# Kernel optimization log

Measured on AMD Instinct MI355X. Metric: run time of the kernel, lower is better.

Reference implementation:

```python
import jax, jax.numpy as jnp
import numpy as np

DIM = 768
HEADS = 12
HIDDEN = 3072  # dim * mlp_ratio
EPS = 1e-5


def layernorm(x, g, b):
    mu = jnp.mean(x, axis=-1, keepdims=True)
    var = jnp.var(x, axis=-1, keepdims=True)
    return (x - mu) * jax.lax.rsqrt(var + EPS) * g + b


def setup_inputs() -> dict:
    key = jax.random.key(0)
    ks = jax.random.split(key, 10)
    s = 0.02
    return {
        "x": jax.random.normal(ks[0], (4, 1024, DIM), jnp.float32),
        "attention_mask": jax.random.randint(ks[1], (4, 1024), 0, 2, jnp.int32),
        "ln1_g": jnp.ones((DIM,), jnp.float32),
        "ln1_b": jnp.zeros((DIM,), jnp.float32),
        "ln2_g": jnp.ones((DIM,), jnp.float32),
        "ln2_b": jnp.zeros((DIM,), jnp.float32),
        "w_qkv": jax.random.normal(ks[2], (DIM, 3 * DIM), jnp.float32) * s,
        "b_qkv": jnp.zeros((3 * DIM,), jnp.float32),
        "w_proj": jax.random.normal(ks[3], (DIM, DIM), jnp.float32) * s,
        "b_proj": jnp.zeros((DIM,), jnp.float32),
        "w_fc1": jax.random.normal(ks[4], (DIM, HIDDEN), jnp.float32) * s,
        "b_fc1": jnp.zeros((HIDDEN,), jnp.float32),
        "w_fc2": jax.random.normal(ks[5], (HIDDEN, DIM), jnp.float32) * s,
        "b_fc2": jnp.zeros((DIM,), jnp.float32),
    }


def reference(x, attention_mask, ln1_g, ln1_b, ln2_g, ln2_b,
              w_qkv, b_qkv, w_proj, b_proj, w_fc1, b_fc1, w_fc2, b_fc2):
    B, N, C = x.shape
    hd = C // HEADS
    scale = hd ** -0.5

    # --- attention branch ---
    h = layernorm(x, ln1_g, ln1_b)
    qkv = (h @ w_qkv + b_qkv).reshape(B, N, 3, HEADS, hd)
    q, k, v = qkv[:, :, 0], qkv[:, :, 1], qkv[:, :, 2]  # [B,N,H,hd]
    attn = jnp.einsum('bnhd,bmhd->bhnm', q, k) * scale
    mask_bias = jnp.where(attention_mask == 0, -10000.0, 0.0)[:, None, None, :]
    attn = jax.nn.softmax(attn + mask_bias, axis=-1)
    o = jnp.einsum('bhnm,bmhd->bnhd', attn, v).reshape(B, N, C)
    x = x + (o @ w_proj + b_proj)

    # --- MLP branch ---
    h = layernorm(x, ln2_g, ln2_b)
    h = jax.nn.gelu(h @ w_fc1 + b_fc1, approximate=False)
    x = x + (h @ w_fc2 + b_fc2)
    return x
```

## Files before the change

### kernel.cpp

```cpp
#include <hip/hip_runtime.h>

#define DIM 768
#define NTOK 4096
#define HID 3072

typedef __attribute__((ext_vector_type(8))) short bf16x8;
typedef __attribute__((ext_vector_type(4))) float f32x4;

__device__ inline unsigned short f2bf(float f){
  unsigned u = __float_as_uint(f);
  u += 0x7fff + ((u >> 16) & 1);
  return (unsigned short)(u >> 16);
}
__device__ inline unsigned cvt_pk_bf16(float a, float b){
  unsigned r;
  asm("v_cvt_pk_bf16_f32 %0, %1, %2" : "=v"(r) : "v"(a), "v"(b));
  return r;
}
__device__ inline void gload_lds16(const void* g, void* l){
  __builtin_amdgcn_global_load_lds(
      (const __attribute__((address_space(1))) unsigned int*)g,
      (__attribute__((address_space(3))) unsigned int*)l, 16, 0, 0);
}
template<int N> __device__ inline void wait_vmcnt(){
  if constexpr (N == 0) asm volatile("s_waitcnt vmcnt(0)" ::: "memory");
  else if constexpr (N == 2) asm volatile("s_waitcnt vmcnt(2)" ::: "memory");
  else if constexpr (N == 3) asm volatile("s_waitcnt vmcnt(3)" ::: "memory");
  else if constexpr (N == 4) asm volatile("s_waitcnt vmcnt(4)" ::: "memory");
  else static_assert(N == 0, "unsupported vmcnt");
}

__global__ __launch_bounds__(256) void ln_kernel(const float* __restrict__ x,
    const float* __restrict__ g, const float* __restrict__ b,
    unsigned short* __restrict__ out)
{
  int row = blockIdx.x * 4 + (threadIdx.x >> 6);
  int lane = threadIdx.x & 63;
  const float* xr = x + (size_t)row * DIM;
  float4 v[3];
  float s = 0.f, s2 = 0.f;
#pragma unroll
  for (int j = 0; j < 3; ++j){
    v[j] = *(const float4*)(xr + j * 256 + lane * 4);
    s  += v[j].x + v[j].y + v[j].z + v[j].w;
    s2 += v[j].x*v[j].x + v[j].y*v[j].y + v[j].z*v[j].z + v[j].w*v[j].w;
  }
#pragma unroll
  for (int m = 1; m < 64; m <<= 1){ s += __shfl_xor(s, m, 64); s2 += __shfl_xor(s2, m, 64); }
  float mu  = s * (1.f / 768.f);
  float var = s2 * (1.f / 768.f) - mu * mu;
  float inv = rsqrtf(var + 1e-5f);
#pragma unroll
  for (int j = 0; j < 3; ++j){
    int c0 = j * 256 + lane * 4;
    float vv[4] = { v[j].x, v[j].y, v[j].z, v[j].w };
    ushort4 o4;
    o4.x = f2bf((vv[0] - mu) * inv * g[c0 + 0] + b[c0 + 0]);
    o4.y = f2bf((vv[1] - mu) * inv * g[c0 + 1] + b[c0 + 1]);
    o4.z = f2bf((vv[2] - mu) * inv * g[c0 + 2] + b[c0 + 2]);
    o4.w = f2bf((vv[3] - mu) * inv * g[c0 + 3] + b[c0 + 3]);
    *(ushort4*)(out + (size_t)row * DIM + c0) = o4;
  }
}

__global__ __launch_bounds__(256) void transpose4_kernel(
    const float* __restrict__ w_qkv, const float* __restrict__ w_proj,
    const float* __restrict__ w_fc1, const float* __restrict__ w_fc2,
    unsigned short* __restrict__ tq, unsigned short* __restrict__ tp,
    unsigned short* __restrict__ t1, unsigned short* __restrict__ t2)
{
  __shared__ __align__(16) unsigned short tile[32][33];
  int id = blockIdx.x;
  const float* W; unsigned short* Wt; int K, N, tx_n;
  if (id < 1728)      { W = w_qkv;  Wt = tq; K = 768;  N = 2304; tx_n = 72; }
  else if (id < 2304) { W = w_proj; Wt = tp; K = 768;  N = 768;  tx_n = 24; id -= 1728; }
  else if (id < 4608) { W = w_fc1;  Wt = t1; K = 768;  N = 3072; tx_n = 96; id -= 2304; }
  else                { W = w_fc2;  Wt = t2; K = 3072; N = 768;  tx_n = 24; id -= 4608; }
  int n0 = (id % tx_n) * 32, k0 = (id / tx_n) * 32;
  int tx = threadIdx.x & 31, ty = threadIdx.x >> 5;
#pragma unroll
  for (int i = 0; i < 32; i += 8)
    tile[ty + i][tx] = f2bf(W[(size_t)(k0 + ty + i) * N + n0 + tx]);
  __syncthreads();
#pragma unroll
  for (int i = 0; i < 32; i += 8)
    Wt[(size_t)(n0 + ty + i) * K + k0 + tx] = tile[tx][ty + i];
}

__global__ __launch_bounds__(256) void pack_mask_kernel(const int* __restrict__ am,
    unsigned long long* __restrict__ pm)
{
  int lane = threadIdx.x & 63, w = threadIdx.x >> 6, b = blockIdx.x;
  for (int k = w; k < 16; k += 4){
    unsigned long long m = __ballot(am[b * 1024 + k * 64 + lane] != 0);
    if (lane == 0) pm[b * 16 + k] = m;
  }
}

template<int BM, int BN, int WM, int WN, int EPI, typename OutT>
__global__ __launch_bounds__(256) void gemm_kernel(
    const unsigned short* __restrict__ A,
    const unsigned short* __restrict__ Bt,
    const float* __restrict__ bias,
    const float* __restrict__ resid,
    OutT* __restrict__ C,
    unsigned short* __restrict__ q_out,
    unsigned short* __restrict__ k_out,
    unsigned short* __restrict__ v_out,
    int M, int N, int K)
{
  constexpr int BK = 32;
  constexpr int WAVES_N = BN / WN;
  constexpr int MI = WM / 16, NI = WN / 16;
  constexpr int ACH = BM * BK / 8, BCH = BN * BK / 8;
  constexpr int NC = (ACH + BCH) / 256;
  constexpr int STAGE_B = 3 * (BM + BN) * BK * 2;
  constexpr int EPI_B = (EPI == 2) ? BM * (BN + 4) * 4 : BM * (BN + 8) * 2;
  constexpr int SMEM_B = STAGE_B > EPI_B ? STAGE_B : EPI_B;
  __shared__ __align__(16) char smem[SMEM_B];
  auto As = (unsigned short(*)[BM * BK])smem;
  auto Bs = (unsigned short(*)[BN * BK])(smem + 3 * BM * BK * 2);
  const int t = threadIdx.x, lane = t & 63, wid = t >> 6;
  const int lo = lane & 15, hi = lane >> 4;
  const int wr = wid / WAVES_N, wc = wid % WAVES_N;

  const int gx = gridDim.x;
  const int nwg = gx * gridDim.y;
  const int lin = blockIdx.y * gx + blockIdx.x;
  const int swz = (lin & 7) * (nwg >> 3) + (lin >> 3);
  const int bm = (swz / gx) * BM, bn = (swz % gx) * BN;

  auto stage = [&](int buf, int k0){
#pragma unroll
    for (int u = 0; u < NC; ++u){
      int c = u * 256 + t;
      if (c < ACH){
        gload_lds16(A + (size_t)(bm + (c >> 2)) * K + k0 + (c & 3) * 8, &As[buf][c * 8]);
      } else {
        int c2 = c - ACH;
        gload_lds16(Bt + (size_t)(bn + (c2 >> 2)) * K + k0 + (c2 & 3) * 8, &Bs[buf][c2 * 8]);
      }
    }
  };

  f32x4 acc[MI][NI];
#pragma unroll
  for (int i = 0; i < MI; ++i)
#pragma unroll
    for (int j = 0; j < NI; ++j) acc[i][j] = (f32x4){0.f, 0.f, 0.f, 0.f};

  const int NIT = K / BK;
  stage(0, 0);
  stage(1, BK);
  for (int it = 0; it < NIT; ++it){
    if (it < NIT - 1) wait_vmcnt<NC>(); else wait_vmcnt<0>();
    __builtin_amdgcn_sched_barrier(0);
    __builtin_amdgcn_s_barrier();
    __builtin_amdgcn_sched_barrier(0);
    if (it + 2 < NIT) stage((it + 2) % 3, (it + 2) * BK);
    const unsigned short* as = As[it % 3];
    const unsigned short* bs = Bs[it % 3];
    bf16x8 af[MI], bfr[NI];
#pragma unroll
    for (int i = 0; i < MI; ++i)  af[i]  = *(const bf16x8*)&as[(wr * WM + i * 16 + lo) * BK + hi * 8];
#pragma unroll
    for (int j = 0; j < NI; ++j) bfr[j] = *(const bf16x8*)&bs[(wc * WN + j * 16 + lo) * BK + hi * 8];
#pragma unroll
    for (int i = 0; i < MI; ++i)
#pragma unroll
      for (int j = 0; j < NI; ++j)
        acc[i][j] = __builtin_amdgcn_mfma_f32_16x16x32_bf16(af[i], bfr[j], acc[i][j], 0, 0, 0);
  }

  __syncthreads();

  if constexpr (EPI == 2){
    constexpr int LDE = BN + 4;
    float* ET = (float*)smem;
#pragma unroll
    for (int i = 0; i < MI; ++i)
#pragma unroll
      for (int j = 0; j < NI; ++j){
        float bcol = bias[bn + wc * WN + j * 16 + lo];
#pragma unroll
        for (int r = 0; r < 4; ++r)
          ET[(wr * WM + i * 16 + hi * 4 + r) * LDE + wc * WN + j * 16 + lo] = acc[i][j][r] + bcol;
      }
    __syncthreads();
    int row = t >> 2, c0 = (t & 3) * 16;
    const float* rrow = resid + (size_t)(bm + row) * N + bn + c0;
    float* crow = (float*)C + (size_t)(bm + row) * N + bn + c0;
#pragma unroll
    for (int k = 0; k < 4; ++k){
      float4 v = *(const float4*)&ET[row * LDE + c0 + k * 4];
      float4 rs = ((const float4*)rrow)[k];
      v.x += rs.x; v.y += rs.y; v.z += rs.z; v.w += rs.w;
      ((float4*)crow)[k] = v;
    }
  } else if constexpr (EPI == 0 || EPI == 1){
    constexpr int LDE = BN + 8;
    unsigned short* ET = (unsigned short*)smem;
#pragma unroll
    for (int i = 0; i < MI; ++i)
#pragma unroll
      for (int j = 0; j < NI; ++j){
        float bcol = bias[bn + wc * WN + j * 16 + lo];
#pragma unroll
        for (int r = 0; r < 4; ++r){
          float v = acc[i][j][r] + bcol;
          if constexpr (EPI == 1) v = 0.5f * v * (1.f + erff(v * 0.70710678118f));
          ET[(wr * WM + i * 16 + hi * 4 + r) * LDE + wc * WN + j * 16 + lo] = f2bf(v);
        }
      }
    __syncthreads();
#pragma unroll
    for (int p = 0; p < BM / 16; ++p){
      int row = p * 16 + (t >> 4), chunk = t & 15;
      if (chunk * 8 < BN)
        *(bf16x8*)&((unsigned short*)C)[(size_t)(bm + row) * N + bn + chunk * 8] =
            *(const bf16x8*)&ET[row * LDE + chunk * 8];
    }
  } else {
    constexpr int LDE = BN + 8;
    unsigned short* ET = (unsigned short*)smem;
    const int part = bn / 768;
    const int cloc = bn % 768;
#pragma unroll
    for (int i = 0; i < MI; ++i)
#pragma unroll
      for (int j = 0; j < NI; ++j){
        int col_l = wc * WN + j * 16 + lo;
        float bcol = bias[bn + col_l];
#pragma unroll
        for (int r = 0; r < 4; ++r){
          int row_l = wr * WM + i * 16 + hi * 4 + r;
          unsigned short us = f2bf(acc[i][j][r] + bcol);
          if (part < 2) ET[row_l * LDE + col_l] = us;
          else          ET[col_l * LDE + row_l] = us;
        }
      }
    __syncthreads();
    const int bb = bm >> 10, n0b = bm & 1023;
    if (part < 2){
      unsigned short* dst0 = (part == 0) ? q_out : k_out;
#pragma unroll
      for (int p = 0; p < 8; ++p){
        int row = p * 16 + (t >> 4), chunk = t & 15;
        int hh = cloc / 64 + (chunk >> 3), d0 = (chunk & 7) * 8;
        unsigned short* dst = dst0 + ((size_t)(bb * 12 + hh)) * 65536 + (n0b + row) * 64 + d0;
        *(bf16x8*)dst = *(const bf16x8*)&ET[row * LDE + chunk * 8];
      }
    } else {
#pragma unroll
      for (int p = 0; p < 8; ++p){
        int colg = p * 16 + (t >> 4), chunk = t & 15;
        int hh = cloc / 64 + (colg >> 6), d = colg & 63;
        unsigned short* dst = v_out + ((size_t)(bb * 12 + hh)) * 65536 + (size_t)d * 1024 + n0b + chunk * 8;
        *(bf16x8*)dst = *(const bf16x8*)&ET[colg * LDE + chunk * 8];
      }
    }
  }
}

__global__ __launch_bounds__(256) void attn_kernel(
    const unsigned short* __restrict__ Qs,
    const unsigned short* __restrict__ Ks,
    const unsigned short* __restrict__ Vts,
    const unsigned long long* __restrict__ pm,
    unsigned short* __restrict__ o)
{
  constexpr int LD = 72;
  __shared__ __align__(16) unsigned short Kl[64 * LD];
  __shared__ __align__(16) unsigned short Vt[64 * LD];
  __shared__ __align__(16) unsigned short Pl[4][16 * LD];
  const int qb = blockIdx.x, h = blockIdx.y, b = blockIdx.z;
  const int t = threadIdx.x, wid = t >> 6, lane = t & 63;
  const int lo = lane & 15, hi = lane >> 4;
  const size_t bh = (size_t)b * 12 + h;

  const unsigned short* Qg = Qs + (bh * 1024 + qb * 64 + wid * 16 + lo) * 64;
  bf16x8 qf0 = *(const bf16x8*)(Qg + hi * 8);
  bf16x8 qf1 = *(const bf16x8*)(Qg + 32 + hi * 8);

  f32x4 oacc[4];
#pragma unroll
  for (int dj = 0; dj < 4; ++dj) oacc[dj] = (f32x4){0.f, 0.f, 0.f, 0.f};
  float l_part = 0.f;

  const int srow = t >> 2, scol = (t & 3) * 16;
  const unsigned short* Kg = Ks  + bh * 65536;
  const unsigned short* Vg = Vts + bh * 65536;
  unsigned short* pw = &Pl[wid][0];

  for (int kt = 0; kt < 16; ++kt){
    __syncthreads();
    const unsigned short* kg = Kg + (kt * 64 + srow) * 64 + scol;
    *(bf16x8*)&Kl[srow * LD + scol]     = *(const bf16x8*)kg;
    *(bf16x8*)&Kl[srow * LD + scol + 8] = *(const bf16x8*)(kg + 8);
    const unsigned short* vg = Vg + srow * 1024 + kt * 64 + scol;
    *(bf16x8*)&Vt[srow * LD + scol]     = *(const bf16x8*)vg;
    *(bf16x8*)&Vt[srow * LD + scol + 8] = *(const bf16x8*)(vg + 8);
    __syncthreads();

    f32x4 s[4];
#pragma unroll
    for (int nj = 0; nj < 4; ++nj) s[nj] = (f32x4){0.f, 0.f, 0.f, 0.f};
#pragma unroll
    for (int kk = 0; kk < 2; ++kk){
      bf16x8 q = kk ? qf1 : qf0;
#pragma unroll
      for (int nj = 0; nj < 4; ++nj){
        bf16x8 kf = *(const bf16x8*)&Kl[(nj * 16 + lo) * LD + kk * 32 + hi * 8];
        s[nj] = __builtin_amdgcn_mfma_f32_16x16x32_bf16(kf, q, s[nj], 0, 0, 0);
      }
    }

    unsigned long long w = pm[b * 16 + kt] >> (hi * 4);
#pragma unroll
    for (int nj = 0; nj < 4; ++nj){
      float p[4];
#pragma unroll
      for (int r = 0; r < 4; ++r){
        float e = __expf(fmaf(s[nj][r], 0.125f, -16.0f));
        e = ((unsigned)(w >> (nj * 16 + r)) & 1u) ? e : 0.0f;
        l_part += e;
        p[r] = e;
      }
      unsigned w0 = cvt_pk_bf16(p[0], p[1]);
      unsigned w1 = cvt_pk_bf16(p[2], p[3]);
      *(uint2*)&pw[lo * LD + nj * 16 + hi * 4] = make_uint2(w0, w1);
    }
    asm volatile("" ::: "memory");
    bf16x8 pf0 = *(const bf16x8*)&pw[lo * LD + hi * 8];
    bf16x8 pf1 = *(const bf16x8*)&pw[lo * LD + 32 + hi * 8];
#pragma unroll
    for (int kk = 0; kk < 2; ++kk){
      bf16x8 pf = kk ? pf1 : pf0;
#pragma unroll
      for (int dj = 0; dj < 4; ++dj){
        bf16x8 vf = *(const bf16x8*)&Vt[(dj * 16 + lo) * LD + kk * 32 + hi * 8];
        oacc[dj] = __builtin_amdgcn_mfma_f32_16x16x32_bf16(vf, pf, oacc[dj], 0, 0, 0);
      }
    }
  }

  float l = l_part;
  l += __shfl_xor(l, 16, 64);
  l += __shfl_xor(l, 32, 64);
  float inv = 1.0f / l;
  size_t orow = (size_t)b * 1024 + qb * 64 + wid * 16 + lo;
#pragma unroll
  for (int dj = 0; dj < 4; ++dj){
    unsigned w0 = (unsigned)f2bf(oacc[dj][0] * inv) | ((unsigned)f2bf(oacc[dj][1] * inv) << 16);
    unsigned w1 = (unsigned)f2bf(oacc[dj][2] * inv) | ((unsigned)f2bf(oacc[dj][3] * inv) << 16);
    *(uint2*)&o[orow * DIM + h * 64 + dj * 16 + hi * 4] = make_uint2(w0, w1);
  }
}

extern "C" void kernel_launch(void* const* d_in, const int* in_sizes, int n_in,
                              void* d_out, int out_size, void* d_ws, size_t ws_size,
                              hipStream_t stream)
{
  const float* x      = (const float*)d_in[0];
  const int*   amask  = (const int*)  d_in[1];
  const float* ln1_g  = (const float*)d_in[2];
  const float* ln1_b  = (const float*)d_in[3];
  const float* ln2_g  = (const float*)d_in[4];
  const float* ln2_b  = (const float*)d_in[5];
  const float* w_qkv  = (const float*)d_in[6];
  const float* b_qkv  = (const float*)d_in[7];
  const float* w_proj = (const float*)d_in[8];
  const float* b_proj = (const float*)d_in[9];
  const float* w_fc1  = (const float*)d_in[10];
  const float* b_fc1  = (const float*)d_in[11];
  const float* w_fc2  = (const float*)d_in[12];
  const float* b_fc2  = (const float*)d_in[13];
  float* outp = (float*)d_out;

  char* w = (char*)d_ws;
  auto alloc = [&](size_t bytes){ char* p = w; w += (bytes + 255) & ~(size_t)255; return p; };

  char* p0 = alloc((size_t)4 * 6291456);
  unsigned short* Qs   = (unsigned short*)p0;
  unsigned short* Ks   = (unsigned short*)(p0 + 6291456);
  unsigned short* Vts  = (unsigned short*)(p0 + 2 * 6291456);
  unsigned short* o_bf = (unsigned short*)(p0 + 3 * 6291456);
  unsigned short* a1   = (unsigned short*)p0;
  unsigned short* h_bf = (unsigned short*)alloc((size_t)NTOK * DIM * 2);
  unsigned short* h2   = h_bf;
  float*          x1   = (float*)alloc((size_t)NTOK * DIM * 4);
  unsigned short* wqkvT = (unsigned short*)alloc((size_t)3 * DIM * DIM * 2);
  unsigned short* wprojT= (unsigned short*)alloc((size_t)DIM * DIM * 2);
  unsigned short* wfc1T = (unsigned short*)alloc((size_t)HID * DIM * 2);
  unsigned short* wfc2T = (unsigned short*)alloc((size_t)DIM * HID * 2);
  unsigned long long* pmask = (unsigned long long*)alloc(4 * 16 * 8);

  transpose4_kernel<<<6912, 256, 0, stream>>>(w_qkv, w_proj, w_fc1, w_fc2,
                                              wqkvT, wprojT, wfc1T, wfc2T);
  pack_mask_kernel<<<4, 256, 0, stream>>>(amask, pmask);

  ln_kernel<<<NTOK / 4, 256, 0, stream>>>(x, ln1_g, ln1_b, h_bf);
  gemm_kernel<128, 128, 64, 64, 3, unsigned short><<<dim3(2304 / 128, NTOK / 128), 256, 0, stream>>>(
      h_bf, wqkvT, b_qkv, nullptr, (unsigned short*)nullptr, Qs, Ks, Vts, NTOK, 2304, DIM);
  attn_kernel<<<dim3(16, 12, 4), 256, 0, stream>>>(Qs, Ks, Vts, pmask, o_bf);
  gemm_kernel<64, 64, 32, 32, 2, float><<<dim3(DIM / 64, NTOK / 64), 256, 0, stream>>>(
      o_bf, wprojT, b_proj, x, x1, nullptr, nullptr, nullptr, NTOK, DIM, DIM);
  ln_kernel<<<NTOK / 4, 256, 0, stream>>>(x1, ln2_g, ln2_b, h2);
  gemm_kernel<128, 128, 64, 64, 1, unsigned short><<<dim3(HID / 128, NTOK / 128), 256, 0, stream>>>(
      h2, wfc1T, b_fc1, nullptr, a1, nullptr, nullptr, nullptr, NTOK, HID, DIM);
  gemm_kernel<64, 64, 32, 32, 2, float><<<dim3(DIM / 64, NTOK / 64), 256, 0, stream>>>(
      a1, wfc2T, b_fc2, x1, outp, nullptr, nullptr, nullptr, NTOK, DIM, HID);
}
```

Before: 185.0 us.

## Use 128x128 tiles with 4-stage pipeline for residual GEMMs

The GEMM kernel is fixed to 128x128 tiles and templated on pipeline depth. The proj and fc2 GEMMs now use 128x128 tiles with a 4-deep load pipeline instead of 64x64 tiles. The fp32 residual epilogue is split into two 64-row halves so its staging buffer fits in the pipeline's shared memory. This raises operand reuse per block, but the grid drops to 192 blocks, which may leave compute units idle.

New measurement: 183.5 us. No clear change (-0.8%).

```diff
diff --git a/kernel.cpp b/kernel.cpp
--- a/kernel.cpp
+++ b/kernel.cpp
@@ -24,9 +24,8 @@
 }
 template<int N> __device__ inline void wait_vmcnt(){
   if constexpr (N == 0) asm volatile("s_waitcnt vmcnt(0)" ::: "memory");
-  else if constexpr (N == 2) asm volatile("s_waitcnt vmcnt(2)" ::: "memory");
-  else if constexpr (N == 3) asm volatile("s_waitcnt vmcnt(3)" ::: "memory");
   else if constexpr (N == 4) asm volatile("s_waitcnt vmcnt(4)" ::: "memory");
+  else if constexpr (N == 8) asm volatile("s_waitcnt vmcnt(8)" ::: "memory");
   else static_assert(N == 0, "unsupported vmcnt");
 }
 
@@ -97,7 +96,7 @@
   }
 }
 
-template<int BM, int BN, int WM, int WN, int EPI, typename OutT>
+template<int DEPTH, int EPI, typename OutT>
 __global__ __launch_bounds__(256) void gemm_kernel(
     const unsigned short* __restrict__ A,
     const unsigned short* __restrict__ Bt,
@@ -109,17 +108,15 @@
     unsigned short* __restrict__ v_out,
     int M, int N, int K)
 {
-  constexpr int BK = 32;
+  constexpr int BM = 128, BN = 128, BK = 32, WM = 64, WN = 64;
   constexpr int WAVES_N = BN / WN;
   constexpr int MI = WM / 16, NI = WN / 16;
   constexpr int ACH = BM * BK / 8, BCH = BN * BK / 8;
   constexpr int NC = (ACH + BCH) / 256;
-  constexpr int STAGE_B = 3 * (BM + BN) * BK * 2;
-  constexpr int EPI_B = (EPI == 2) ? BM * (BN + 4) * 4 : BM * (BN + 8) * 2;
-  constexpr int SMEM_B = STAGE_B > EPI_B ? STAGE_B : EPI_B;
+  constexpr int SMEM_B = DEPTH * (BM + BN) * BK * 2;
   __shared__ __align__(16) char smem[SMEM_B];
   auto As = (unsigned short(*)[BM * BK])smem;
-  auto Bs = (unsigned short(*)[BN * BK])(smem + 3 * BM * BK * 2);
+  auto Bs = (unsigned short(*)[BN * BK])(smem + DEPTH * BM * BK * 2);
   const int t = threadIdx.x, lane = t & 63, wid = t >> 6;
   const int lo = lane & 15, hi = lane >> 4;
   const int wr = wid / WAVES_N, wc = wid % WAVES_N;
@@ -150,16 +147,19 @@
     for (int j = 0; j < NI; ++j) acc[i][j] = (f32x4){0.f, 0.f, 0.f, 0.f};
 
   const int NIT = K / BK;
-  stage(0, 0);
-  stage(1, BK);
+#pragma unroll
+  for (int d = 0; d < DEPTH - 1; ++d) stage(d, d * BK);
   for (int it = 0; it < NIT; ++it){
-    if (it < NIT - 1) wait_vmcnt<NC>(); else wait_vmcnt<0>();
+    int rem = NIT - 1 - it;
+    if (rem >= DEPTH - 2) wait_vmcnt<(DEPTH - 2) * NC>();
+    else if (DEPTH == 4 && rem == 1) wait_vmcnt<NC>();
+    else wait_vmcnt<0>();
     __builtin_amdgcn_sched_barrier(0);
     __builtin_amdgcn_s_barrier();
     __builtin_amdgcn_sched_barrier(0);
-    if (it + 2 < NIT) stage((it + 2) % 3, (it + 2) * BK);
-    const unsigned short* as = As[it % 3];
-    const unsigned short* bs = Bs[it % 3];
+    if (it + DEPTH - 1 < NIT) stage((it + DEPTH - 1) % DEPTH, (it + DEPTH - 1) * BK);
+    const unsigned short* as = As[it % DEPTH];
+    const unsigned short* bs = Bs[it % DEPTH];
     bf16x8 af[MI], bfr[NI];
 #pragma unroll
     for (int i = 0; i < MI; ++i)  af[i]  = *(const bf16x8*)&as[(wr * WM + i * 16 + lo) * BK + hi * 8];
@@ -178,24 +178,31 @@
     constexpr int LDE = BN + 4;
     float* ET = (float*)smem;
 #pragma unroll
-    for (int i = 0; i < MI; ++i)
-#pragma unroll
-      for (int j = 0; j < NI; ++j){
-        float bcol = bias[bn + wc * WN + j * 16 + lo];
-#pragma unroll
-        for (int r = 0; r < 4; ++r)
-          ET[(wr * WM + i * 16 + hi * 4 + r) * LDE + wc * WN + j * 16 + lo] = acc[i][j][r] + bcol;
-      }
-    __syncthreads();
-    int row = t >> 2, c0 = (t & 3) * 16;
-    const float* rrow = resid + (size_t)(bm + row) * N + bn + c0;
-    float* crow = (float*)C + (size_t)(bm + row) * N + bn + c0;
-#pragma unroll
-    for (int k = 0; k < 4; ++k){
-      float4 v = *(const float4*)&ET[row * LDE + c0 + k * 4];
-      float4 rs = ((const float4*)rrow)[k];
-      v.x += rs.x; v.y += rs.y; v.z += rs.z; v.w += rs.w;
-      ((float4*)crow)[k] = v;
+    for (int half = 0; half < 2; ++half){
+      if (wr == half){
+#pragma unroll
+        for (int i = 0; i < MI; ++i)
+#pragma unroll
+          for (int j = 0; j < NI; ++j){
+            float bcol = bias[bn + wc * WN + j * 16 + lo];
+#pragma unroll
+            for (int r = 0; r < 4; ++r)
+              ET[(i * 16 + hi * 4 + r) * LDE + wc * WN + j * 16 + lo] = acc[i][j][r] + bcol;
+          }
+      }
+      __syncthreads();
+      int lrow = t >> 2, gg = t & 3;
+      const float* rrow = resid + (size_t)(bm + half * 64 + lrow) * N + bn;
+      float* crow = (float*)C + (size_t)(bm + half * 64 + lrow) * N + bn;
+#pragma unroll
+      for (int k = 0; k < 8; ++k){
+        int c4 = (gg + k * 4) * 4;
+        float4 v = *(const float4*)&ET[lrow * LDE + c4];
+        float4 rs = *(const float4*)&rrow[c4];
+        v.x += rs.x; v.y += rs.y; v.z += rs.z; v.w += rs.w;
+        *(float4*)&crow[c4] = v;
+      }
+      if (half == 0) __syncthreads();
     }
   } else if constexpr (EPI == 0 || EPI == 1){
     constexpr int LDE = BN + 8;
@@ -216,9 +223,8 @@
 #pragma unroll
     for (int p = 0; p < BM / 16; ++p){
       int row = p * 16 + (t >> 4), chunk = t & 15;
-      if (chunk * 8 < BN)
-        *(bf16x8*)&((unsigned short*)C)[(size_t)(bm + row) * N + bn + chunk * 8] =
-            *(const bf16x8*)&ET[row * LDE + chunk * 8];
+      *(bf16x8*)&((unsigned short*)C)[(size_t)(bm + row) * N + bn + chunk * 8] =
+          *(const bf16x8*)&ET[row * LDE + chunk * 8];
     }
   } else {
     constexpr int LDE = BN + 8;
@@ -400,14 +406,14 @@
   pack_mask_kernel<<<4, 256, 0, stream>>>(amask, pmask);
 
   ln_kernel<<<NTOK / 4, 256, 0, stream>>>(x, ln1_g, ln1_b, h_bf);
-  gemm_kernel<128, 128, 64, 64, 3, unsigned short><<<dim3(2304 / 128, NTOK / 128), 256, 0, stream>>>(
+  gemm_kernel<3, 3, unsigned short><<<dim3(2304 / 128, NTOK / 128), 256, 0, stream>>>(
       h_bf, wqkvT, b_qkv, nullptr, (unsigned short*)nullptr, Qs, Ks, Vts, NTOK, 2304, DIM);
   attn_kernel<<<dim3(16, 12, 4), 256, 0, stream>>>(Qs, Ks, Vts, pmask, o_bf);
-  gemm_kernel<64, 64, 32, 32, 2, float><<<dim3(DIM / 64, NTOK / 64), 256, 0, stream>>>(
+  gemm_kernel<4, 2, float><<<dim3(DIM / 128, NTOK / 128), 256, 0, stream>>>(
       o_bf, wprojT, b_proj, x, x1, nullptr, nullptr, nullptr, NTOK, DIM, DIM);
   ln_kernel<<<NTOK / 4, 256, 0, stream>>>(x1, ln2_g, ln2_b, h2);
-  gemm_kernel<128, 128, 64, 64, 1, unsigned short><<<dim3(HID / 128, NTOK / 128), 256, 0, stream>>>(
+  gemm_kernel<3, 1, unsigned short><<<dim3(HID / 128, NTOK / 128), 256, 0, stream>>>(
       h2, wfc1T, b_fc1, nullptr, a1, nullptr, nullptr, nullptr, NTOK, HID, DIM);
-  gemm_kernel<64, 64, 32, 32, 2, float><<<dim3(DIM / 64, NTOK / 64), 256, 0, stream>>>(
+  gemm_kernel<4, 2, float><<<dim3(DIM / 128, NTOK / 128), 256, 0, stream>>>(
       a1, wfc2T, b_fc2, x1, outp, nullptr, nullptr, nullptr, NTOK, DIM, HID);
 }
```
